# Performance work log

Measured on AMD Instinct MI355X. Metric: run time of the kernel, lower is better.

## Reference

```python
import jax, jax.numpy as jnp
import numpy as np

HIDDEN = 4096
N_HEADS = 32
N_KV_HEADS = 8
HEAD_DIM = HIDDEN // N_HEADS  # 128
GROUPS = N_HEADS // N_KV_HEADS  # 4
ATTN_MULT = 0.08838834764831845  # 1/sqrt(head_dim)
MAX_ATTN_VAL = 30.0
NEG_INF = -1e30


def setup_inputs() -> dict:
    key = jax.random.key(0)
    ks = jax.random.split(key, 5)
    B, S = 2, 2048
    hidden_states = jax.random.normal(ks[0], (B, S, HIDDEN), dtype=jnp.float32)
    scale = 1.0 / np.sqrt(HIDDEN)
    Wq = jax.random.normal(ks[1], (HIDDEN, N_HEADS * HEAD_DIM), dtype=jnp.float32) * scale
    Wk = jax.random.normal(ks[2], (HIDDEN, N_KV_HEADS * HEAD_DIM), dtype=jnp.float32) * scale
    Wv = jax.random.normal(ks[3], (HIDDEN, N_KV_HEADS * HEAD_DIM), dtype=jnp.float32) * scale
    Wo = jax.random.normal(ks[4], (N_HEADS * HEAD_DIM, HIDDEN), dtype=jnp.float32) * scale
    return {"hidden_states": hidden_states, "Wq": Wq, "Wk": Wk, "Wv": Wv, "Wo": Wo}


def reference(hidden_states, Wq, Wk, Wv, Wo):
    B, S, _ = hidden_states.shape
    # projections
    q = (hidden_states @ Wq).reshape(B, S, N_HEADS, HEAD_DIM).transpose(0, 2, 1, 3)      # bhsd
    k = (hidden_states @ Wk).reshape(B, S, N_KV_HEADS, HEAD_DIM).transpose(0, 2, 1, 3)   # bksd
    v = (hidden_states @ Wv).reshape(B, S, N_KV_HEADS, HEAD_DIM).transpose(0, 2, 1, 3)
    # GQA: expand kv heads to query heads
    k = jnp.repeat(k, GROUPS, axis=1)  # [B, N_HEADS, S, D]
    v = jnp.repeat(v, GROUPS, axis=1)
    # scaled scores with Grok-style tanh soft-cap
    scores = jnp.einsum('bhqd,bhkd->bhqk', q, k) * ATTN_MULT
    scores = MAX_ATTN_VAL * jnp.tanh(scores / MAX_ATTN_VAL)
    # causal mask
    causal = jnp.tril(jnp.ones((S, S), dtype=bool))
    scores = jnp.where(causal[None, None], scores, NEG_INF)
    probs = jax.nn.softmax(scores.astype(jnp.float32), axis=-1).astype(v.dtype)
    out = jnp.einsum('bhqk,bhkd->bhqd', probs, v)          # [B, H, S, D]
    out = out.transpose(0, 2, 1, 3).reshape(B, S, N_HEADS * HEAD_DIM)
    return out @ Wo
```

## Files before the change

kernel.cpp:

```cpp
#include <hip/hip_runtime.h>
#include <hip/hip_bf16.h>
#include <type_traits>
#include <cmath>

#define HIDDEN 4096
#define NHEADS 32
#define NKV 8
#define HD 128
#define BB 2
#define SS 2048
#define NTOK (BB*SS)
#define ATTN_MULT 0.08838834764831845f

using bf16x8 = __attribute__((ext_vector_type(8))) short;
using f32x4  = __attribute__((ext_vector_type(4))) float;

using gas = __attribute__((address_space(1))) const void;
using las = __attribute__((address_space(3))) void;

__device__ __forceinline__ unsigned short f2bf(float f){
  unsigned int u = __builtin_bit_cast(unsigned int, f);
  u += 0x7fffu + ((u >> 16) & 1u);
  return (unsigned short)(u >> 16);
}

__global__ void cvt_f32_bf16_k(const float* __restrict__ in, unsigned short* __restrict__ out, int n8){
  int i = blockIdx.x * blockDim.x + threadIdx.x;
  if (i >= n8) return;
  const float4* p = (const float4*)in + (size_t)i * 2;
  float4 a = p[0], b = p[1];
  bf16x8 o;
  o[0]=f2bf(a.x); o[1]=f2bf(a.y); o[2]=f2bf(a.z); o[3]=f2bf(a.w);
  o[4]=f2bf(b.x); o[5]=f2bf(b.y); o[6]=f2bf(b.z); o[7]=f2bf(b.w);
  ((bf16x8*)out)[i] = o;
}

__global__ void transpose_cvt_k(const float* __restrict__ W, unsigned short* __restrict__ WT, int K, int N){
  __shared__ float tile[32][33];
  int n0 = blockIdx.x * 32, k0 = blockIdx.y * 32;
  int tx = threadIdx.x, ty = threadIdx.y;
  #pragma unroll
  for (int i = 0; i < 4; ++i)
    tile[ty*4+i][tx] = W[(size_t)(k0 + ty*4 + i) * N + n0 + tx];
  __syncthreads();
  #pragma unroll
  for (int i = 0; i < 4; ++i)
    WT[(size_t)(n0 + ty*4 + i) * K + k0 + tx] = f2bf(tile[tx][ty*4+i]);
}

__global__ void transpose_v_k(const unsigned short* __restrict__ in, unsigned short* __restrict__ out){
  __shared__ unsigned short tile[32][33];
  int c0 = blockIdx.x * 32, r0 = blockIdx.y * 32;
  int tx = threadIdx.x, ty = threadIdx.y;
  #pragma unroll
  for (int i = 0; i < 4; ++i)
    tile[ty*4+i][tx] = in[(size_t)(r0 + ty*4 + i) * 2048 + 1024 + c0 + tx];
  __syncthreads();
  #pragma unroll
  for (int i = 0; i < 4; ++i){
    int c = c0 + ty*4 + i, r = r0 + tx;
    out[((size_t)((r >> 11) * 1024 + c)) * 2048 + (r & 2047)] = tile[tx][ty*4+i];
  }
}

template<typename OutT>
__global__ __launch_bounds__(256, 3)
void gemm_bt_k(const unsigned short* __restrict__ A,
               const unsigned short* __restrict__ BT,
               OutT* __restrict__ C, int M, int N, int K){
  __shared__ __align__(16) unsigned short As[128*32];
  __shared__ __align__(16) unsigned short Bs[128*32];
  const int m0 = blockIdx.y * 128, n0 = blockIdx.x * 128;
  const int tid = threadIdx.x, w = tid >> 6, lane = tid & 63;
  const int wr = w >> 1, wc = w & 1;
  const int lrow = lane & 15, lk = (lane >> 4) * 8;
  const int arow = lane >> 2, acol = (lane & 3) * 8;

  f32x4 acc[4][4] = {};

  for (int k0 = 0; k0 < K; k0 += 32){
    #pragma unroll
    for (int i = 0; i < 2; ++i){
      int chunk = w*2 + i;
      const unsigned short* ga = A  + (size_t)(m0 + chunk*16 + arow) * K + k0 + acol;
      const unsigned short* gb = BT + (size_t)(n0 + chunk*16 + arow) * K + k0 + acol;
      __builtin_amdgcn_global_load_lds((gas*)ga, (las*)(As + chunk*512), 16, 0, 0);
      __builtin_amdgcn_global_load_lds((gas*)gb, (las*)(Bs + chunk*512), 16, 0, 0);
    }
    __syncthreads();
    bf16x8 af[4], bfr[4];
    #pragma unroll
    for (int m = 0; m < 4; ++m) af[m]  = *(const bf16x8*)&As[(wr*64 + m*16 + lrow)*32 + lk];
    #pragma unroll
    for (int n = 0; n < 4; ++n) bfr[n] = *(const bf16x8*)&Bs[(wc*64 + n*16 + lrow)*32 + lk];
    #pragma unroll
    for (int m = 0; m < 4; ++m)
      #pragma unroll
      for (int n = 0; n < 4; ++n)
        acc[m][n] = __builtin_amdgcn_mfma_f32_16x16x32_bf16(af[m], bfr[n], acc[m][n], 0, 0, 0);
    __syncthreads();
  }

  const int crow = (lane >> 4) * 4, ccol = lane & 15;
  #pragma unroll
  for (int m = 0; m < 4; ++m)
    #pragma unroll
    for (int n = 0; n < 4; ++n){
      size_t base = (size_t)(m0 + wr*64 + m*16 + crow) * N + n0 + wc*64 + n*16 + ccol;
      #pragma unroll
      for (int r = 0; r < 4; ++r){
        float v = acc[m][n][r];
        if constexpr (std::is_same<OutT, unsigned short>::value) C[base + (size_t)r*N] = f2bf(v);
        else                                                     C[base + (size_t)r*N] = v;
      }
    }
}

#define GBAR() asm volatile("s_barrier" ::: "memory")

#define GEMM_PHASE(P, VMN, STAGE_STMT)                                          \
  {                                                                             \
    bf16x8 af[2][2];                                                            \
    _Pragma("unroll") for (int mi = 0; mi < 2; ++mi)                            \
    _Pragma("unroll") for (int kk = 0; kk < 2; ++kk){                           \
      int row = wm*128 + (P)*32 + mi*16 + lrow;                                 \
      int c8 = (kk*4 + lhi) ^ (row & 7);                                        \
      af[mi][kk] = *(const bf16x8*)&As[cur][row*64 + c8*8];                     \
    }                                                                           \
    if ((P) == 0){                                                              \
      _Pragma("unroll") for (int nf = 0; nf < 4; ++nf)                          \
      _Pragma("unroll") for (int kk = 0; kk < 2; ++kk){                         \
        int row = wn*64 + nf*16 + lrow;                                         \
        int c8 = (kk*4 + lhi) ^ (row & 7);                                      \
        bf[nf][kk] = *(const bf16x8*)&Bs[cur][row*64 + c8*8];                   \
      }                                                                         \
    }                                                                           \
    STAGE_STMT;                                                                 \
    asm volatile("s_waitcnt vmcnt(" #VMN ")");                                  \
    GBAR();                                                                     \
    __builtin_amdgcn_s_setprio(1);                                              \
    _Pragma("unroll") for (int mi = 0; mi < 2; ++mi)                            \
    _Pragma("unroll") for (int nf = 0; nf < 4; ++nf)                            \
    _Pragma("unroll") for (int kk = 0; kk < 2; ++kk)                            \
      acc[(P)*2+mi][nf] = __builtin_amdgcn_mfma_f32_16x16x32_bf16(              \
          af[mi][kk], bf[nf][kk], acc[(P)*2+mi][nf], 0, 0, 0);                  \
    __builtin_amdgcn_s_setprio(0);                                              \
    GBAR();                                                                     \
  }

template<typename OutT>
__global__ __launch_bounds__(512, 2)
void gemm8_k(const unsigned short* __restrict__ A,
             const unsigned short* __restrict__ BT,
             OutT* __restrict__ C, int M, int N, int K){
  __shared__ __align__(16) unsigned short As[2][256*64];
  __shared__ __align__(16) unsigned short Bs[2][256*64];

  const int nbx = N >> 8;
  const int id = blockIdx.x + blockIdx.y * nbx;
  const int nwg = nbx * (M >> 8);
  const int swz = (id & 7) * (nwg >> 3) + (id >> 3);
  const int m0 = (swz / nbx) << 8, n0 = (swz % nbx) << 8;

  const int tid = threadIdx.x, w = tid >> 6, lane = tid & 63;
  const int wm = w >> 2, wn = w & 3;
  const int lrow = lane & 15, lhi = lane >> 4;
  const int l3 = lane >> 3, k8l = lane & 7;
  const int NT = K >> 6;

  f32x4 acc[8][4] = {};
  bf16x8 bf[4][2];

  auto stageB = [&](int t, int s, int half){
    #pragma unroll
    for (int j = 0; j < 2; ++j){
      int row0 = half*128 + j*64 + w*8;
      int row = row0 + l3;
      const unsigned short* g = BT + (size_t)(n0 + row) * K + t*64 + ((k8l ^ (row & 7)) << 3);
      __builtin_amdgcn_global_load_lds((gas*)g, (las*)(&Bs[s][0] + row0*64), 16, 0, 0);
    }
  };
  auto stageA = [&](int t, int s, int g2){
    #pragma unroll
    for (int j = 0; j < 2; ++j){
      int g = g2 + j;
      int row0 = ((w >= 4) ? 128 : 0) + g*32 + (w & 3)*8;
      int row = row0 + l3;
      const unsigned short* ga = A + (size_t)(m0 + row) * K + t*64 + ((k8l ^ (row & 7)) << 3);
      __builtin_amdgcn_global_load_lds((gas*)ga, (las*)(&As[s][0] + row0*64), 16, 0, 0);
    }
  };

  stageB(0, 0, 0); stageB(0, 0, 1); stageA(0, 0, 0); stageA(0, 0, 2);
  asm volatile("s_waitcnt vmcnt(3)");
  GBAR();

  for (int t = 0; t < NT - 1; ++t){
    const int cur = t & 1, nxt = cur ^ 1;
    GEMM_PHASE(0, 4, stageB(t+1, nxt, 0));
    GEMM_PHASE(1, 5, stageB(t+1, nxt, 1));
    GEMM_PHASE(2, 6, stageA(t+1, nxt, 0));
    GEMM_PHASE(3, 3, stageA(t+1, nxt, 2));
  }
  {
    const int cur = (NT - 1) & 1;
    GEMM_PHASE(0, 2, (void)0);
    GEMM_PHASE(1, 1, (void)0);
    GEMM_PHASE(2, 0, (void)0);
    GEMM_PHASE(3, 0, (void)0);
  }

  #pragma unroll
  for (int mf = 0; mf < 8; ++mf)
    #pragma unroll
    for (int nf = 0; nf < 4; ++nf){
      size_t base = (size_t)(m0 + wm*128 + mf*16 + lhi*4) * N + n0 + wn*64 + nf*16 + lrow;
      #pragma unroll
      for (int r = 0; r < 4; ++r){
        float v = acc[mf][nf][r];
        if constexpr (std::is_same<OutT, unsigned short>::value) C[base + (size_t)r*N] = f2bf(v);
        else                                                     C[base + (size_t)r*N] = v;
      }
    }
}

__global__ __launch_bounds__(512, 2)
void attn_k(const unsigned short* __restrict__ Q,
            const unsigned short* __restrict__ KVp,
            const unsigned short* __restrict__ VTp,
            unsigned short* __restrict__ ctx){
  __shared__ __align__(16) unsigned short Ks[2][64*128];
  __shared__ __align__(16) unsigned short Vt[2][128*64];
  __shared__ __align__(16) unsigned short Ps[8][32*32];

  const int Wb = blockIdx.x;
  const int xcd = Wb & 7, sI = Wb >> 3;
  const int idx = sI & 31, half = sI >> 5;
  const int a = idx & 3;
  const int qt = half ? a : 7 - a;
  const int hs = (idx >> 2) & 3, gsub = (idx >> 4) & 1;
  const int group = xcd*2 + gsub;
  const int b = group >> 3, kvh = group & 7;
  const int h = kvh*4 + hs;

  const int tid = threadIdx.x, w = tid >> 6, lane = tid & 63;
  const int q0 = qt * 256;
  const int nt = 4*qt + 4;
  const int lrow = lane & 15, lhi = lane >> 4;
  const int qwb = q0 + w*32;

  bf16x8 qf[2][4];
  {
    const unsigned short* qb = Q + (size_t)(b*SS + qwb + lrow) * 4096 + h*HD + lhi*8;
    #pragma unroll
    for (int qg = 0; qg < 2; ++qg)
      #pragma unroll
      for (int ks = 0; ks < 4; ++ks)
        qf[qg][ks] = *(const bf16x8*)(qb + (size_t)qg*16*4096 + ks*32);
  }

  f32x4 o[8][2] = {};
  float psum[8] = {};

  const unsigned short* Kbh  = KVp + (size_t)b * SS * 2048 + kvh * HD;
  const unsigned short* VTbh = VTp + ((size_t)b * 1024 + kvh * HD) * SS;

  auto STAGE = [&](int db, int t){
    #pragma unroll
    for (int it = 0; it < 2; ++it){
      int cbase = it*512 + w*64;
      int c = cbase + lane;
      int kkv = c >> 4, kc = c & 15;
      const unsigned short* gk = Kbh + (size_t)(t*64 + kkv) * 2048 + ((kc ^ (kkv & 7)) << 3);
      __builtin_amdgcn_global_load_lds((gas*)gk, (las*)(&Ks[db][0] + cbase*8), 16, 0, 0);
      int vd = c >> 3, vc = c & 7;
      const unsigned short* gv = VTbh + (size_t)vd * SS + t*64 + ((vc ^ ((vd ^ (vd >> 3)) & 7)) << 3);
      __builtin_amdgcn_global_load_lds((gas*)gv, (las*)(&Vt[db][0] + cbase*8), 16, 0, 0);
    }
  };

  STAGE(0, 0);
  __syncthreads();

  for (int t = 0; t < nt; ++t){
    const int db = t & 1;
    if (t + 1 < nt) STAGE(db ^ 1, t + 1);

    if (t*64 <= qwb + 31){
      const char* Kc = (const char*)&Ks[db][0];
      const char* Vc = (const char*)&Vt[db][0];
      unsigned short* Pw = &Ps[w][0];

      #pragma unroll
      for (int hh = 0; hh < 2; ++hh){
        #pragma unroll
        for (int cc = 0; cc < 2; ++cc){
          const int cf = hh*2 + cc;
          const int row = cf*16 + lrow;
          bf16x8 kf[4];
          #pragma unroll
          for (int ks = 0; ks < 4; ++ks){
            int kbyte = (row*256 + (ks*32 + lhi*8)*2) ^ ((row & 7) << 4);
            kf[ks] = *(const bf16x8*)(Kc + kbyte);
          }
          f32x4 s0 = {0.f,0.f,0.f,0.f}, s1 = {0.f,0.f,0.f,0.f};
          #pragma unroll
          for (int ks = 0; ks < 4; ++ks){
            s0 = __builtin_amdgcn_mfma_f32_16x16x32_bf16(qf[0][ks], kf[ks], s0, 0, 0, 0);
            s1 = __builtin_amdgcn_mfma_f32_16x16x32_bf16(qf[1][ks], kf[ks], s1, 0, 0, 0);
          }
          const int kvg = t*64 + cf*16 + lrow;
          const int colh = cc*16 + lrow;
          #pragma unroll
          for (int qg = 0; qg < 2; ++qg){
            #pragma unroll
            for (int r = 0; r < 4; ++r){
              float sc = (qg ? s1[r] : s0[r]) * ATTN_MULT;
              float e  = __expf(sc * (2.f/30.f));
              float ex = -60.f * __builtin_amdgcn_rcpf(e + 1.f);
              int qglob = qwb + qg*16 + lhi*4 + r;
              float p = (kvg <= qglob) ? __expf(ex) : 0.f;
              psum[qg*4 + r] += p;
              int prow = qg*16 + lhi*4 + r;
              int pbyte = prow*64 + ((colh*2) ^ (((prow >> 2) & 3) << 4));
              *(unsigned short*)((char*)Pw + pbyte) = f2bf(p);
            }
          }
        }
        bf16x8 pf[2];
        #pragma unroll
        for (int qg = 0; qg < 2; ++qg){
          int prow = qg*16 + lrow;
          int pbyte = prow*64 + ((lhi*16) ^ (((prow >> 2) & 3) << 4));
          pf[qg] = *(const bf16x8*)((char*)Pw + pbyte);
        }
        #pragma unroll
        for (int df = 0; df < 8; ++df){
          int d = df*16 + lrow;
          int vbyte = (d*128 + (hh*32 + lhi*8)*2) ^ (((d ^ (d >> 3)) & 7) << 4);
          bf16x8 vf = *(const bf16x8*)(Vc + vbyte);
          o[df][0] = __builtin_amdgcn_mfma_f32_16x16x32_bf16(pf[0], vf, o[df][0], 0, 0, 0);
          o[df][1] = __builtin_amdgcn_mfma_f32_16x16x32_bf16(pf[1], vf, o[df][1], 0, 0, 0);
        }
      }
    }
    __syncthreads();
  }

  #pragma unroll
  for (int qg = 0; qg < 2; ++qg){
    #pragma unroll
    for (int r = 0; r < 4; ++r){
      float sum = psum[qg*4 + r];
      sum += __shfl_xor(sum, 1);
      sum += __shfl_xor(sum, 2);
      sum += __shfl_xor(sum, 4);
      sum += __shfl_xor(sum, 8);
      float inv = 1.f / sum;
      size_t base = (size_t)(b*SS + qwb + qg*16 + lhi*4 + r) * 4096 + h*HD + lrow;
      #pragma unroll
      for (int df = 0; df < 8; ++df)
        ctx[base + df*16] = f2bf(o[df][qg][r] * inv);
    }
  }
}

#define O_HSB   ((size_t)0)
#define O_WQT   ((size_t)33554432)
#define O_WKT   ((size_t)67108864)
#define O_WVT   ((size_t)75497472)
#define O_WOT   ((size_t)83886080)
#define O_Q     ((size_t)117440512)
#define O_KV    ((size_t)150994944)
#define O_CTX   ((size_t)167772160)
#define WS_NEED ((size_t)201326592)

extern "C" void kernel_launch(void* const* d_in, const int* in_sizes, int n_in,
                              void* d_out, int out_size, void* d_ws, size_t ws_size,
                              hipStream_t stream){
  if (ws_size < WS_NEED) return;
  const float* hs = (const float*)d_in[0];
  const float* Wq = (const float*)d_in[1];
  const float* Wk = (const float*)d_in[2];
  const float* Wv = (const float*)d_in[3];
  const float* Wo = (const float*)d_in[4];
  char* ws = (char*)d_ws;
  unsigned short* hsb = (unsigned short*)(ws + O_HSB);
  unsigned short* WqT = (unsigned short*)(ws + O_WQT);
  unsigned short* WkT = (unsigned short*)(ws + O_WKT);
  unsigned short* WvT = (unsigned short*)(ws + O_WVT);
  unsigned short* WoT = (unsigned short*)(ws + O_WOT);
  unsigned short* Qb  = (unsigned short*)(ws + O_Q);
  unsigned short* KVb = (unsigned short*)(ws + O_KV);
  unsigned short* ctxb= (unsigned short*)(ws + O_CTX);
  unsigned short* VTb = (unsigned short*)(ws + O_WQT);

  cvt_f32_bf16_k<<<dim3((NTOK*HIDDEN/8)/256), dim3(256), 0, stream>>>(hs, hsb, NTOK*HIDDEN/8);
  transpose_cvt_k<<<dim3(128,128), dim3(32,8), 0, stream>>>(Wq, WqT, 4096, 4096);
  transpose_cvt_k<<<dim3(32,128),  dim3(32,8), 0, stream>>>(Wk, WkT, 4096, 1024);
  transpose_cvt_k<<<dim3(32,128),  dim3(32,8), 0, stream>>>(Wv, WvT, 4096, 1024);
  transpose_cvt_k<<<dim3(128,128), dim3(32,8), 0, stream>>>(Wo, WoT, 4096, 4096);
  gemm8_k<unsigned short><<<dim3(16,16), dim3(512), 0, stream>>>(hsb, WqT, Qb, 4096, 4096, 4096);
  gemm_bt_k<unsigned short><<<dim3(16,32), dim3(256), 0, stream>>>(hsb, WkT, KVb, 4096, 2048, 4096);
  transpose_v_k<<<dim3(32,128), dim3(32,8), 0, stream>>>(KVb, VTb);
  attn_k<<<dim3(512), dim3(512), 0, stream>>>(Qb, KVb, VTb, ctxb);
  gemm8_k<float><<<dim3(16,16), dim3(512), 0, stream>>>(ctxb, WoT, (float*)d_out, 4096, 4096, 4096);
}
```

Before: 585.1 us.

## Transpose attention MFMA operands, polynomial softcap, packed bf16 P stores

The QK^T and PV MFMAs now run with swapped operands, so each lane holds consecutive kv columns for one query row. That lets P be written to LDS as packed 4-element bf16 stores using v_cvt_pk_bf16_f32, with a new swizzle and a larger per-warp P buffer. The whole 64-wide score tile is computed before softmax, and the row-sum reduction shrinks to two shuffles. The tanh soft-cap plus exp becomes a clamped odd polynomial approximation followed by a single exp, and the context output is written as packed 4-wide stores. This adds LDS footprint and register pressure, and the polynomial tanh approximation risks accuracy at large scores.

```diff
diff --git a/kernel.cpp b/kernel.cpp
--- a/kernel.cpp
+++ b/kernel.cpp
@@ -22,6 +22,11 @@
   unsigned int u = __builtin_bit_cast(unsigned int, f);
   u += 0x7fffu + ((u >> 16) & 1u);
   return (unsigned short)(u >> 16);
+}
+__device__ __forceinline__ unsigned int cvtpk(float lo, float hi){
+  unsigned int r;
+  asm("v_cvt_pk_bf16_f32 %0, %1, %2" : "=v"(r) : "v"(lo), "v"(hi));
+  return r;
 }
 
 __global__ void cvt_f32_bf16_k(const float* __restrict__ in, unsigned short* __restrict__ out, int n8){
@@ -231,7 +236,7 @@
             unsigned short* __restrict__ ctx){
   __shared__ __align__(16) unsigned short Ks[2][64*128];
   __shared__ __align__(16) unsigned short Vt[2][128*64];
-  __shared__ __align__(16) unsigned short Ps[8][32*32];
+  __shared__ __align__(16) unsigned short Ps[8][2048];
 
   const int Wb = blockIdx.x;
   const int xcd = Wb & 7, sI = Wb >> 3;
@@ -248,6 +253,7 @@
   const int nt = 4*qt + 4;
   const int lrow = lane & 15, lhi = lane >> 4;
   const int qwb = q0 + w*32;
+  const int xorv = (lrow & 7) << 4;
 
   bf16x8 qf[2][4];
   {
@@ -260,7 +266,7 @@
   }
 
   f32x4 o[8][2] = {};
-  float psum[8] = {};
+  float psum[2] = {0.f, 0.f};
 
   const unsigned short* Kbh  = KVp + (size_t)b * SS * 2048 + kvh * HD;
   const unsigned short* VTbh = VTp + ((size_t)b * 1024 + kvh * HD) * SS;
@@ -289,58 +295,64 @@
     if (t*64 <= qwb + 31){
       const char* Kc = (const char*)&Ks[db][0];
       const char* Vc = (const char*)&Vt[db][0];
-      unsigned short* Pw = &Ps[w][0];
+      char* Pw = (char*)&Ps[w][0];
+
+      f32x4 sacc[2][4];
+      #pragma unroll
+      for (int cf = 0; cf < 4; ++cf){
+        const int row = cf*16 + lrow;
+        bf16x8 kf[4];
+        #pragma unroll
+        for (int ks = 0; ks < 4; ++ks){
+          int kbyte = (row*256 + (ks*32 + lhi*8)*2) ^ ((row & 7) << 4);
+          kf[ks] = *(const bf16x8*)(Kc + kbyte);
+        }
+        f32x4 s0 = {0.f,0.f,0.f,0.f}, s1 = {0.f,0.f,0.f,0.f};
+        #pragma unroll
+        for (int ks = 0; ks < 4; ++ks){
+          s0 = __builtin_amdgcn_mfma_f32_16x16x32_bf16(kf[ks], qf[0][ks], s0, 0, 0, 0);
+          s1 = __builtin_amdgcn_mfma_f32_16x16x32_bf16(kf[ks], qf[1][ks], s1, 0, 0, 0);
+        }
+        sacc[0][cf] = s0; sacc[1][cf] = s1;
+      }
+
+      #pragma unroll
+      for (int qg = 0; qg < 2; ++qg){
+        const int qglob = qwb + qg*16 + lrow;
+        #pragma unroll
+        for (int cf = 0; cf < 4; ++cf){
+          float pv[4];
+          #pragma unroll
+          for (int r = 0; r < 4; ++r){
+            float s = sacc[qg][cf][r] * ATTN_MULT;
+            s = fminf(fmaxf(s, -25.f), 25.f);
+            float s2 = s*s;
+            float wv = __builtin_fmaf(s2, -3.7037037e-4f, 1.f);
+            wv = __builtin_fmaf(s2*s2, 1.6460905e-7f, wv);
+            float tt = s * wv;
+            int kvg = t*64 + cf*16 + lhi*4 + r;
+            float p = (kvg <= qglob) ? __expf(tt - 30.f) : 0.f;
+            psum[qg] += p;
+            pv[r] = p;
+          }
+          uint2 pk;
+          pk.x = cvtpk(pv[0], pv[1]);
+          pk.y = cvtpk(pv[2], pv[3]);
+          *(uint2*)(Pw + qg*2048 + lrow*128 + ((cf*32 + lhi*8) ^ xorv)) = pk;
+        }
+      }
 
       #pragma unroll
       for (int hh = 0; hh < 2; ++hh){
-        #pragma unroll
-        for (int cc = 0; cc < 2; ++cc){
-          const int cf = hh*2 + cc;
-          const int row = cf*16 + lrow;
-          bf16x8 kf[4];
-          #pragma unroll
-          for (int ks = 0; ks < 4; ++ks){
-            int kbyte = (row*256 + (ks*32 + lhi*8)*2) ^ ((row & 7) << 4);
-            kf[ks] = *(const bf16x8*)(Kc + kbyte);
-          }
-          f32x4 s0 = {0.f,0.f,0.f,0.f}, s1 = {0.f,0.f,0.f,0.f};
-          #pragma unroll
-          for (int ks = 0; ks < 4; ++ks){
-            s0 = __builtin_amdgcn_mfma_f32_16x16x32_bf16(qf[0][ks], kf[ks], s0, 0, 0, 0);
-            s1 = __builtin_amdgcn_mfma_f32_16x16x32_bf16(qf[1][ks], kf[ks], s1, 0, 0, 0);
-          }
-          const int kvg = t*64 + cf*16 + lrow;
-          const int colh = cc*16 + lrow;
-          #pragma unroll
-          for (int qg = 0; qg < 2; ++qg){
-            #pragma unroll
-            for (int r = 0; r < 4; ++r){
-              float sc = (qg ? s1[r] : s0[r]) * ATTN_MULT;
-              float e  = __expf(sc * (2.f/30.f));
-              float ex = -60.f * __builtin_amdgcn_rcpf(e + 1.f);
-              int qglob = qwb + qg*16 + lhi*4 + r;
-              float p = (kvg <= qglob) ? __expf(ex) : 0.f;
-              psum[qg*4 + r] += p;
-              int prow = qg*16 + lhi*4 + r;
-              int pbyte = prow*64 + ((colh*2) ^ (((prow >> 2) & 3) << 4));
-              *(unsigned short*)((char*)Pw + pbyte) = f2bf(p);
-            }
-          }
-        }
-        bf16x8 pf[2];
-        #pragma unroll
-        for (int qg = 0; qg < 2; ++qg){
-          int prow = qg*16 + lrow;
-          int pbyte = prow*64 + ((lhi*16) ^ (((prow >> 2) & 3) << 4));
-          pf[qg] = *(const bf16x8*)((char*)Pw + pbyte);
-        }
+        bf16x8 pf0 = *(const bf16x8*)(Pw +        lrow*128 + ((hh*64 + lhi*16) ^ xorv));
+        bf16x8 pf1 = *(const bf16x8*)(Pw + 2048 + lrow*128 + ((hh*64 + lhi*16) ^ xorv));
         #pragma unroll
         for (int df = 0; df < 8; ++df){
           int d = df*16 + lrow;
           int vbyte = (d*128 + (hh*32 + lhi*8)*2) ^ (((d ^ (d >> 3)) & 7) << 4);
           bf16x8 vf = *(const bf16x8*)(Vc + vbyte);
-          o[df][0] = __builtin_amdgcn_mfma_f32_16x16x32_bf16(pf[0], vf, o[df][0], 0, 0, 0);
-          o[df][1] = __builtin_amdgcn_mfma_f32_16x16x32_bf16(pf[1], vf, o[df][1], 0, 0, 0);
+          o[df][0] = __builtin_amdgcn_mfma_f32_16x16x32_bf16(vf, pf0, o[df][0], 0, 0, 0);
+          o[df][1] = __builtin_amdgcn_mfma_f32_16x16x32_bf16(vf, pf1, o[df][1], 0, 0, 0);
         }
       }
     }
@@ -349,18 +361,17 @@
 
   #pragma unroll
   for (int qg = 0; qg < 2; ++qg){
-    #pragma unroll
-    for (int r = 0; r < 4; ++r){
-      float sum = psum[qg*4 + r];
-      sum += __shfl_xor(sum, 1);
-      sum += __shfl_xor(sum, 2);
-      sum += __shfl_xor(sum, 4);
-      sum += __shfl_xor(sum, 8);
-      float inv = 1.f / sum;
-      size_t base = (size_t)(b*SS + qwb + qg*16 + lhi*4 + r) * 4096 + h*HD + lrow;
-      #pragma unroll
-      for (int df = 0; df < 8; ++df)
-        ctx[base + df*16] = f2bf(o[df][qg][r] * inv);
+    float sum = psum[qg];
+    sum += __shfl_xor(sum, 16);
+    sum += __shfl_xor(sum, 32);
+    float inv = 1.f / sum;
+    unsigned short* base = ctx + (size_t)(b*SS + qwb + qg*16 + lrow) * 4096 + h*HD + lhi*4;
+    #pragma unroll
+    for (int df = 0; df < 8; ++df){
+      uint2 pk;
+      pk.x = cvtpk(o[df][qg][0] * inv, o[df][qg][1] * inv);
+      pk.y = cvtpk(o[df][qg][2] * inv, o[df][qg][3] * inv);
+      *(uint2*)(base + df*16) = pk;
     }
   }
 }
```

Result: faster. 570.3 us (-2.5%).
